# Kernel tuning notes

Measured on AMD Instinct MI355X. Metric: run time of the kernel, lower is better.

Reference implementation:

```python
import jax, jax.numpy as jnp
import numpy as np

B, F, D, L, N = 2048, 40, 64, 3, 40  # batch, num_fields, embed_dim, num_layers, num_subspaces


def setup_inputs() -> dict:
    key = jax.random.key(0)
    inputs = jax.random.normal(key, (B, F, D), dtype=jnp.float32)
    # Parameters per layer, matching torch init exactly:
    #   W     = identity(D) repeated over out_subspaces -> [N, D, D]
    #   alpha = ones([num_fields, in_subspaces, out_subspaces]); in_subspaces == F for
    #           layer 0 and == N afterwards; with N == F all layers share shape [F, N, N]
    #   h     = ones([N, D, 1])
    W = jnp.broadcast_to(jnp.eye(D, dtype=jnp.float32), (L, N, D, D)).copy()
    alpha = jnp.ones((L, F, N, N), dtype=jnp.float32)
    h = jnp.ones((L, N, D, 1), dtype=jnp.float32)
    return {"inputs": inputs, "W": W, "alpha": alpha, "h": h}


def _fusion_layer(B0, Bi, W, alpha, h):
    # Original math: fusion[b,n,D,d] = sum_{f,i} alpha[f,i,n] * B0[b,f,D] * Bi[b,i,d]
    #                out[b,n,D]     = sum_d fusion[b,n,D,d] * W[n,D,d] * h[n,d]
    # Reordered to avoid the [b,f,n,D,d] outer-product tensor:
    M = W * h[:, :, 0][:, None, :]                 # [n, D, d] = W * h broadcast over D
    C = jnp.einsum('bid,nDd->binD', Bi, M)         # contract embed dim d first
    out = jnp.einsum('bfD,fin,binD->bnD', B0, alpha, C)
    return out


def reference(inputs, W, alpha, h):
    B_i = inputs
    for l in range(L):
        B_i = _fusion_layer(inputs, B_i, W[l], alpha[l], h[l])
    return B_i
```

## Files before the change

### kernel.cpp

```cpp
#include <hip/hip_runtime.h>


typedef __bf16 bf16x8 __attribute__((ext_vector_type(8)));
typedef float  f32x16 __attribute__((ext_vector_type(16)));
typedef unsigned short us4 __attribute__((ext_vector_type(4)));

constexpr int BATCH = 2048;
constexpr int FDIM  = 40;
constexpr int DDIM  = 64;
constexpr int LAY   = 3;
constexpr int IPAD  = 64;
constexpr int FPAD  = 48;
constexpr int NSPL  = 4;
constexpr int NPB   = FDIM / NSPL;

__device__ __forceinline__ unsigned short f2bf(float f) {
  union { float f; unsigned u; } v; v.f = f;
  unsigned r = v.u + 0x7fff + ((v.u >> 16) & 1);
  return (unsigned short)(r >> 16);
}

__global__ void prep_k(const float* __restrict__ W, const float* __restrict__ h,
                       const float* __restrict__ alpha, const float* __restrict__ inputs,
                       unsigned short* __restrict__ M, unsigned short* __restrict__ AT,
                       unsigned short* __restrict__ B0b, unsigned short* __restrict__ B0T) {
  int j = blockIdx.x * blockDim.x + threadIdx.x;
  const int nM4 = LAY * FDIM * DDIM * DDIM / 4;
  const int nA4 = LAY * FDIM * IPAD * FPAD / 4;
  const int nB4 = BATCH * FDIM * DDIM / 4;
  const int nT4 = BATCH * DDIM * FPAD / 4;
  if (j < nM4) {
    int e  = j * 4;
    int d  = e & 63;
    int ln = e >> 12;
    float4 wv = *reinterpret_cast<const float4*>(W + e);
    float4 hv = *reinterpret_cast<const float4*>(h + ln * DDIM + d);
    us4 o = { f2bf(wv.x * hv.x), f2bf(wv.y * hv.y), f2bf(wv.z * hv.z), f2bf(wv.w * hv.w) };
    *reinterpret_cast<us4*>(M + e) = o;
    return;
  }
  j -= nM4;
  if (j < nA4) {
    int e  = j * 4;
    int f  = e % FPAD;
    int ii = (e / FPAD) % IPAD;
    int n  = (e / (FPAD * IPAD)) % FDIM;
    int l  = e / (FPAD * IPAD * FDIM);
    us4 o = {0, 0, 0, 0};
    if (ii < FDIM) {
#pragma unroll
      for (int k = 0; k < 4; ++k)
        if (f + k < FDIM)
          o[k] = f2bf(alpha[(((size_t)l * FDIM + f + k) * FDIM + ii) * FDIM + n]);
    }
    *reinterpret_cast<us4*>(AT + e) = o;
    return;
  }
  j -= nA4;
  if (j < nB4) {
    int e = j * 4;
    float4 v = *reinterpret_cast<const float4*>(inputs + e);
    us4 o = { f2bf(v.x), f2bf(v.y), f2bf(v.z), f2bf(v.w) };
    *reinterpret_cast<us4*>(B0b + e) = o;
    return;
  }
  j -= nB4;
  if (j >= nT4) return;
  {
    int e  = j * 4;
    int f  = e % FPAD;
    int d  = (e / FPAD) % DDIM;
    int b  = e / (FPAD * DDIM);
    us4 o = {0, 0, 0, 0};
#pragma unroll
    for (int k = 0; k < 4; ++k)
      if (f + k < FDIM)
        o[k] = f2bf(inputs[((size_t)b * FDIM + f + k) * DDIM + d]);
    *reinterpret_cast<us4*>(B0T + e) = o;
  }
}

template <bool FINAL>
__global__ __launch_bounds__(128, 2) void layer_k(
    const unsigned short* __restrict__ Bi,
    const unsigned short* __restrict__ B0T,
    const unsigned short* __restrict__ Mt,
    const unsigned short* __restrict__ ATt,
    void* __restrict__ outp)
{
  const int tid  = threadIdx.x;
  const int lane = tid & 63;
  const int w    = tid >> 6;
  const int c    = lane & 31;
  const int h    = lane >> 5;
  const int bg   = blockIdx.x >> 2;
  const int nBase = (blockIdx.x & 3) * NPB;
  const int bb   = bg * 4 + w * 2;

  bf16x8 aBi[2][2][4];
#pragma unroll
  for (int b2 = 0; b2 < 2; ++b2)
#pragma unroll
    for (int it = 0; it < 2; ++it) {
      int row = it * 32 + c; if (row > FDIM - 1) row = FDIM - 1;
#pragma unroll
      for (int ks = 0; ks < 4; ++ks)
        aBi[b2][it][ks] = *reinterpret_cast<const bf16x8*>(
            Bi + ((size_t)(bb + b2) * FDIM + row) * DDIM + ks * 16 + h * 8);
    }

  bf16x8 bT[2][2][3];
#pragma unroll
  for (int b2 = 0; b2 < 2; ++b2)
#pragma unroll
    for (int dt = 0; dt < 2; ++dt)
#pragma unroll
      for (int ks = 0; ks < 3; ++ks)
        bT[b2][dt][ks] = *reinterpret_cast<const bf16x8*>(
            B0T + ((size_t)(bb + b2) * DDIM + dt * 32 + c) * FPAD + ks * 16 + h * 8);

  for (int ln = 0; ln < NPB; ++ln) {
    const int n = nBase + ln;
    const unsigned short* Mn = Mt  + n * (DDIM * DDIM);
    const unsigned short* An = ATt + n * (IPAD * FPAD);

    bf16x8 mb[2][4];
#pragma unroll
    for (int dt = 0; dt < 2; ++dt)
#pragma unroll
      for (int ks = 0; ks < 4; ++ks)
        mb[dt][ks] = *reinterpret_cast<const bf16x8*>(
            Mn + (dt * 32 + c) * DDIM + ks * 16 + h * 8);

    bf16x8 at[2][3];
#pragma unroll
    for (int it = 0; it < 2; ++it)
#pragma unroll
      for (int ks = 0; ks < 3; ++ks)
        at[it][ks] = *reinterpret_cast<const bf16x8*>(
            An + (it * 32 + c) * FPAD + ks * 16 + h * 8);

    float pout[2][2] = {{0.f, 0.f}, {0.f, 0.f}};

#pragma unroll
    for (int it = 0; it < 2; ++it) {
#pragma unroll
      for (int dt = 0; dt < 2; ++dt) {
        f32x16 aC0 = {0,0,0,0,0,0,0,0,0,0,0,0,0,0,0,0};
        f32x16 aC1 = {0,0,0,0,0,0,0,0,0,0,0,0,0,0,0,0};
        f32x16 aR0 = {0,0,0,0,0,0,0,0,0,0,0,0,0,0,0,0};
        f32x16 aR1 = {0,0,0,0,0,0,0,0,0,0,0,0,0,0,0,0};
#pragma unroll
        for (int ks = 0; ks < 4; ++ks) {
          aC0 = __builtin_amdgcn_mfma_f32_32x32x16_bf16(aBi[0][it][ks], mb[dt][ks], aC0, 0, 0, 0);
          aC1 = __builtin_amdgcn_mfma_f32_32x32x16_bf16(aBi[1][it][ks], mb[dt][ks], aC1, 0, 0, 0);
        }
#pragma unroll
        for (int ks = 0; ks < 3; ++ks) {
          aR0 = __builtin_amdgcn_mfma_f32_32x32x16_bf16(at[it][ks], bT[0][dt][ks], aR0, 0, 0, 0);
          aR1 = __builtin_amdgcn_mfma_f32_32x32x16_bf16(at[it][ks], bT[1][dt][ks], aR1, 0, 0, 0);
        }
        {
          float t0 = 0.f, t1 = 0.f, t2 = 0.f, t3 = 0.f;
#pragma unroll
          for (int r = 0; r < 4; ++r) {
            t0 += aC0[r] * aR0[r];         t1 += aC0[r + 4] * aR0[r + 4];
            t2 += aC0[r + 8] * aR0[r + 8]; t3 += aC0[r + 12] * aR0[r + 12];
          }
          pout[0][dt] += (t0 + t1) + (t2 + t3);
        }
        {
          float t0 = 0.f, t1 = 0.f, t2 = 0.f, t3 = 0.f;
#pragma unroll
          for (int r = 0; r < 4; ++r) {
            t0 += aC1[r] * aR1[r];         t1 += aC1[r + 4] * aR1[r + 4];
            t2 += aC1[r + 8] * aR1[r + 8]; t3 += aC1[r + 12] * aR1[r + 12];
          }
          pout[1][dt] += (t0 + t1) + (t2 + t3);
        }
      }
    }

#pragma unroll
    for (int b2 = 0; b2 < 2; ++b2) {
      float v0 = pout[b2][0] + __shfl_xor(pout[b2][0], 32, 64);
      float v1 = pout[b2][1] + __shfl_xor(pout[b2][1], 32, 64);
      float val = h ? v1 : v0;
      size_t off = ((size_t)(bb + b2) * FDIM + n) * DDIM + lane;
      if (FINAL) ((float*)outp)[off] = val;
      else       ((unsigned short*)outp)[off] = f2bf(val);
    }
  }
}

extern "C" void kernel_launch(void* const* d_in, const int* in_sizes, int n_in,
                              void* d_out, int out_size, void* d_ws, size_t ws_size,
                              hipStream_t stream) {
  const float* inputs = (const float*)d_in[0];
  const float* W      = (const float*)d_in[1];
  const float* alpha  = (const float*)d_in[2];
  const float* h      = (const float*)d_in[3];

  char* ws = (char*)d_ws;
  const size_t S   = (size_t)BATCH * FDIM * DDIM * 2;
  const size_t ST  = (size_t)BATCH * DDIM * FPAD * 2;
  unsigned short* Bi1 = (unsigned short*)(ws);
  unsigned short* Bi2 = (unsigned short*)(ws + S);
  unsigned short* B0b = (unsigned short*)(ws + 2 * S);
  unsigned short* B0T = (unsigned short*)(ws + 3 * S);
  unsigned short* Mb  = (unsigned short*)(ws + 3 * S + ST);
  unsigned short* ATb = (unsigned short*)(ws + 3 * S + ST + (size_t)LAY * FDIM * DDIM * DDIM * 2);

  const int nPrep4 = (LAY * FDIM * DDIM * DDIM + LAY * FDIM * IPAD * FPAD
                    + BATCH * FDIM * DDIM + BATCH * DDIM * FPAD) / 4;
  prep_k<<<(nPrep4 + 255) / 256, 256, 0, stream>>>(W, h, alpha, inputs, Mb, ATb, B0b, B0T);

  dim3 grid(BATCH / 4 * NSPL), blk(128);
  const size_t mL = (size_t)FDIM * DDIM * DDIM;
  const size_t aL = (size_t)FDIM * IPAD * FPAD;
  layer_k<false><<<grid, blk, 0, stream>>>(B0b, B0T, Mb, ATb, Bi1);
  layer_k<false><<<grid, blk, 0, stream>>>(Bi1, B0T, Mb + mL, ATb + aL, Bi2);
  layer_k<true ><<<grid, blk, 0, stream>>>(Bi2, B0T, Mb + 2 * mL, ATb + 2 * aL, d_out);
}
```

Before: 263.2 us.

## Fuse all three layers into one kernel with per-wave LDS intermediate

Replaces three per-layer launches with a single kernel where each wave processes one batch row through all layers, keeping the intermediate Bi in shared memory rather than global workspace. This removes launch overhead and global round trips of intermediate activations. In exchange, weight tiles are no longer reused across two batch rows per wave and total wave count halves, lowering parallelism and increasing per-wave serial work.

```diff
diff --git a/kernel.cpp b/kernel.cpp
--- a/kernel.cpp
+++ b/kernel.cpp
@@ -11,8 +11,7 @@
 constexpr int LAY   = 3;
 constexpr int IPAD  = 64;
 constexpr int FPAD  = 48;
-constexpr int NSPL  = 4;
-constexpr int NPB   = FDIM / NSPL;
+constexpr int LROW  = 72;
 
 __device__ __forceinline__ unsigned short f2bf(float f) {
   union { float f; unsigned u; } v; v.f = f;
@@ -80,85 +79,91 @@
   }
 }
 
-template <bool FINAL>
-__global__ __launch_bounds__(128, 2) void layer_k(
-    const unsigned short* __restrict__ Bi,
+__global__ __launch_bounds__(128, 2) void fused_k(
+    const unsigned short* __restrict__ B0b,
     const unsigned short* __restrict__ B0T,
     const unsigned short* __restrict__ Mt,
     const unsigned short* __restrict__ ATt,
-    void* __restrict__ outp)
+    float* __restrict__ outp)
 {
+  __shared__ __align__(16) unsigned short xpose[2][FDIM * LROW];
+
   const int tid  = threadIdx.x;
   const int lane = tid & 63;
   const int w    = tid >> 6;
   const int c    = lane & 31;
   const int h    = lane >> 5;
-  const int bg   = blockIdx.x >> 2;
-  const int nBase = (blockIdx.x & 3) * NPB;
-  const int bb   = bg * 4 + w * 2;
-
-  bf16x8 aBi[2][2][4];
-#pragma unroll
-  for (int b2 = 0; b2 < 2; ++b2)
-#pragma unroll
-    for (int it = 0; it < 2; ++it) {
-      int row = it * 32 + c; if (row > FDIM - 1) row = FDIM - 1;
-#pragma unroll
-      for (int ks = 0; ks < 4; ++ks)
-        aBi[b2][it][ks] = *reinterpret_cast<const bf16x8*>(
-            Bi + ((size_t)(bb + b2) * FDIM + row) * DDIM + ks * 16 + h * 8);
+  const int b    = blockIdx.x * 2 + w;
+  unsigned short* myL = xpose[w];
+
+  bf16x8 bT[2][3];
+#pragma unroll
+  for (int dt = 0; dt < 2; ++dt)
+#pragma unroll
+    for (int ks = 0; ks < 3; ++ks)
+      bT[dt][ks] = *reinterpret_cast<const bf16x8*>(
+          B0T + ((size_t)b * DDIM + dt * 32 + c) * FPAD + ks * 16 + h * 8);
+
+  bf16x8 aBi[2][4];
+#pragma unroll
+  for (int it = 0; it < 2; ++it) {
+    int row = it * 32 + c; if (row > FDIM - 1) row = FDIM - 1;
+#pragma unroll
+    for (int ks = 0; ks < 4; ++ks)
+      aBi[it][ks] = *reinterpret_cast<const bf16x8*>(
+          B0b + ((size_t)b * FDIM + row) * DDIM + ks * 16 + h * 8);
+  }
+
+  for (int l = 0; l < LAY; ++l) {
+    const unsigned short* Ml = Mt  + l * (FDIM * DDIM * DDIM);
+    const unsigned short* Al = ATt + l * (FDIM * IPAD * FPAD);
+
+    if (l > 0) {
+#pragma unroll
+      for (int it = 0; it < 2; ++it) {
+        int row = it * 32 + c; if (row > FDIM - 1) row = FDIM - 1;
+#pragma unroll
+        for (int ks = 0; ks < 4; ++ks)
+          aBi[it][ks] = *reinterpret_cast<const bf16x8*>(
+              (const char*)myL + row * (LROW * 2) + ks * 32 + h * 16);
+      }
     }
 
-  bf16x8 bT[2][2][3];
-#pragma unroll
-  for (int b2 = 0; b2 < 2; ++b2)
-#pragma unroll
-    for (int dt = 0; dt < 2; ++dt)
-#pragma unroll
-      for (int ks = 0; ks < 3; ++ks)
-        bT[b2][dt][ks] = *reinterpret_cast<const bf16x8*>(
-            B0T + ((size_t)(bb + b2) * DDIM + dt * 32 + c) * FPAD + ks * 16 + h * 8);
-
-  for (int ln = 0; ln < NPB; ++ln) {
-    const int n = nBase + ln;
-    const unsigned short* Mn = Mt  + n * (DDIM * DDIM);
-    const unsigned short* An = ATt + n * (IPAD * FPAD);
-
-    bf16x8 mb[2][4];
-#pragma unroll
-    for (int dt = 0; dt < 2; ++dt)
-#pragma unroll
-      for (int ks = 0; ks < 4; ++ks)
-        mb[dt][ks] = *reinterpret_cast<const bf16x8*>(
-            Mn + (dt * 32 + c) * DDIM + ks * 16 + h * 8);
-
-    bf16x8 at[2][3];
-#pragma unroll
-    for (int it = 0; it < 2; ++it)
-#pragma unroll
-      for (int ks = 0; ks < 3; ++ks)
-        at[it][ks] = *reinterpret_cast<const bf16x8*>(
-            An + (it * 32 + c) * FPAD + ks * 16 + h * 8);
-
-    float pout[2][2] = {{0.f, 0.f}, {0.f, 0.f}};
-
-#pragma unroll
-    for (int it = 0; it < 2; ++it) {
-#pragma unroll
-      for (int dt = 0; dt < 2; ++dt) {
+    for (int n = 0; n < FDIM; ++n) {
+      const unsigned short* Mn = Ml + n * (DDIM * DDIM);
+      const unsigned short* An = Al + n * (IPAD * FPAD);
+
+      bf16x8 mb[2][4];
+#pragma unroll
+      for (int dt = 0; dt < 2; ++dt)
+#pragma unroll
+        for (int ks = 0; ks < 4; ++ks)
+          mb[dt][ks] = *reinterpret_cast<const bf16x8*>(
+              Mn + (dt * 32 + c) * DDIM + ks * 16 + h * 8);
+      bf16x8 at[2][3];
+#pragma unroll
+      for (int it = 0; it < 2; ++it)
+#pragma unroll
+        for (int ks = 0; ks < 3; ++ks)
+          at[it][ks] = *reinterpret_cast<const bf16x8*>(
+              An + (it * 32 + c) * FPAD + ks * 16 + h * 8);
+
+      float pout[2] = {0.f, 0.f};
+#pragma unroll
+      for (int it = 0; it < 2; ++it) {
         f32x16 aC0 = {0,0,0,0,0,0,0,0,0,0,0,0,0,0,0,0};
         f32x16 aC1 = {0,0,0,0,0,0,0,0,0,0,0,0,0,0,0,0};
         f32x16 aR0 = {0,0,0,0,0,0,0,0,0,0,0,0,0,0,0,0};
         f32x16 aR1 = {0,0,0,0,0,0,0,0,0,0,0,0,0,0,0,0};
 #pragma unroll
         for (int ks = 0; ks < 4; ++ks) {
-          aC0 = __builtin_amdgcn_mfma_f32_32x32x16_bf16(aBi[0][it][ks], mb[dt][ks], aC0, 0, 0, 0);
-          aC1 = __builtin_amdgcn_mfma_f32_32x32x16_bf16(aBi[1][it][ks], mb[dt][ks], aC1, 0, 0, 0);
+          aC0 = __builtin_amdgcn_mfma_f32_32x32x16_bf16(aBi[it][ks], mb[0][ks], aC0, 0, 0, 0);
+          aC1 = __builtin_amdgcn_mfma_f32_32x32x16_bf16(aBi[it][ks], mb[1][ks], aC1, 0, 0, 0);
         }
 #pragma unroll
         for (int ks = 0; ks < 3; ++ks) {
-          aR0 = __builtin_amdgcn_mfma_f32_32x32x16_bf16(at[it][ks], bT[0][dt][ks], aR0, 0, 0, 0);
-          aR1 = __builtin_amdgcn_mfma_f32_32x32x16_bf16(at[it][ks], bT[1][dt][ks], aR1, 0, 0, 0);
+          aR0 = __builtin_amdgcn_mfma_f32_32x32x16_bf16(at[it][ks], bT[0][ks], aR0, 0, 0, 0);
+          aR1 = __builtin_amdgcn_mfma_f32_32x32x16_bf16(at[it][ks], bT[1][ks], aR1, 0, 0, 0);
         }
         {
           float t0 = 0.f, t1 = 0.f, t2 = 0.f, t3 = 0.f;
@@ -167,7 +172,7 @@
             t0 += aC0[r] * aR0[r];         t1 += aC0[r + 4] * aR0[r + 4];
             t2 += aC0[r + 8] * aR0[r + 8]; t3 += aC0[r + 12] * aR0[r + 12];
           }
-          pout[0][dt] += (t0 + t1) + (t2 + t3);
+          pout[0] += (t0 + t1) + (t2 + t3);
         }
         {
           float t0 = 0.f, t1 = 0.f, t2 = 0.f, t3 = 0.f;
@@ -176,19 +181,18 @@
             t0 += aC1[r] * aR1[r];         t1 += aC1[r + 4] * aR1[r + 4];
             t2 += aC1[r + 8] * aR1[r + 8]; t3 += aC1[r + 12] * aR1[r + 12];
           }
-          pout[1][dt] += (t0 + t1) + (t2 + t3);
+          pout[1] += (t0 + t1) + (t2 + t3);
         }
       }
-    }
-
-#pragma unroll
-    for (int b2 = 0; b2 < 2; ++b2) {
-      float v0 = pout[b2][0] + __shfl_xor(pout[b2][0], 32, 64);
-      float v1 = pout[b2][1] + __shfl_xor(pout[b2][1], 32, 64);
+
+      float v0 = pout[0] + __shfl_xor(pout[0], 32, 64);
+      float v1 = pout[1] + __shfl_xor(pout[1], 32, 64);
       float val = h ? v1 : v0;
-      size_t off = ((size_t)(bb + b2) * FDIM + n) * DDIM + lane;
-      if (FINAL) ((float*)outp)[off] = val;
-      else       ((unsigned short*)outp)[off] = f2bf(val);
+      if (l == LAY - 1) {
+        outp[((size_t)b * FDIM + n) * DDIM + lane] = val;
+      } else {
+        myL[n * LROW + lane] = f2bf(val);
+      }
     }
   }
 }
@@ -204,21 +208,14 @@
   char* ws = (char*)d_ws;
   const size_t S   = (size_t)BATCH * FDIM * DDIM * 2;
   const size_t ST  = (size_t)BATCH * DDIM * FPAD * 2;
-  unsigned short* Bi1 = (unsigned short*)(ws);
-  unsigned short* Bi2 = (unsigned short*)(ws + S);
-  unsigned short* B0b = (unsigned short*)(ws + 2 * S);
-  unsigned short* B0T = (unsigned short*)(ws + 3 * S);
-  unsigned short* Mb  = (unsigned short*)(ws + 3 * S + ST);
-  unsigned short* ATb = (unsigned short*)(ws + 3 * S + ST + (size_t)LAY * FDIM * DDIM * DDIM * 2);
+  unsigned short* B0b = (unsigned short*)(ws);
+  unsigned short* B0T = (unsigned short*)(ws + S);
+  unsigned short* Mb  = (unsigned short*)(ws + S + ST);
+  unsigned short* ATb = (unsigned short*)(ws + S + ST + (size_t)LAY * FDIM * DDIM * DDIM * 2);
 
   const int nPrep4 = (LAY * FDIM * DDIM * DDIM + LAY * FDIM * IPAD * FPAD
                     + BATCH * FDIM * DDIM + BATCH * DDIM * FPAD) / 4;
   prep_k<<<(nPrep4 + 255) / 256, 256, 0, stream>>>(W, h, alpha, inputs, Mb, ATb, B0b, B0T);
 
-  dim3 grid(BATCH / 4 * NSPL), blk(128);
-  const size_t mL = (size_t)FDIM * DDIM * DDIM;
-  const size_t aL = (size_t)FDIM * IPAD * FPAD;
-  layer_k<false><<<grid, blk, 0, stream>>>(B0b, B0T, Mb, ATb, Bi1);
-  layer_k<false><<<grid, blk, 0, stream>>>(Bi1, B0T, Mb + mL, ATb + aL, Bi2);
-  layer_k<true ><<<grid, blk, 0, stream>>>(Bi2, B0T, Mb + 2 * mL, ATb + 2 * aL, d_out);
-}
+  fused_k<<<dim3(BATCH / 2), dim3(128), 0, stream>>>(B0b, B0T, Mb, ATb, (float*)d_out);
+}
```

Measured after the change: 359.9 us. 1.37x slower.
